# Kernel tuning notes

Hardware: AMD Instinct MI355X
Metric: run time of the kernel (lower is better)

Reference implementation:

```python
import jax, jax.numpy as jnp
import numpy as np

B, T, E, H = 4, 1024, 1024, 16
DH = E // H  # 64
LTM, CM0, CM1, MEM = 1, 512, 256, 1024
KV = LTM + CM0 + CM1 + MEM + T  # 2817


def _shift(x):
    # relative-position shift trick; x: [..., i, j] -> [..., i, j]
    *pre, i, j = x.shape
    x = jnp.concatenate([x, jnp.zeros((*pre, i, i), x.dtype)], axis=-1)
    l = i + j - 1
    x = x.reshape(*pre, -1)
    pad = (-x.shape[-1]) % l
    x = jnp.concatenate([x, jnp.zeros((*pre, pad), x.dtype)], axis=-1)
    x = x.reshape(*pre, -1, l)
    return x[..., :i, i - 1:]


def setup_inputs() -> dict:
    key = jax.random.key(0)
    ks = jax.random.split(key, 10)
    return {
        'x': jax.random.normal(ks[0], (B, T, E), jnp.float32),
        'mem': jax.random.normal(ks[1], (B, MEM, E), jnp.float32),
        'cmem0': jax.random.normal(ks[2], (B, CM0, E), jnp.float32),
        'cmem1': jax.random.normal(ks[3], (B, CM1, E), jnp.float32),
        'ltmem': jax.random.normal(ks[4], (B, LTM, E), jnp.float32),
        'pos_emb': jax.random.normal(ks[5], (H, KV, DH), jnp.float32) * 0.02,
        'Wq': jax.random.normal(ks[6], (E, E), jnp.float32) * 0.02,
        'Wkv': jax.random.normal(ks[7], (2 * E, E), jnp.float32) * 0.02,
        'Wout': jax.random.normal(ks[8], (E, E), jnp.float32) * 0.02,
        'bout': jnp.zeros((E,), jnp.float32),
    }


def reference(x, mem, cmem0, cmem1, ltmem, pos_emb, Wq, Wkv, Wout, bout):
    b, t, e = x.shape
    scale = DH ** -0.5
    # kv input: (ltmem, *cmems, mem, x) along sequence dim
    kv_input = jnp.concatenate([ltmem, cmem0, cmem1, mem, x], axis=1)
    kv_len = kv_input.shape[1]
    total_mem_len = kv_len - t

    q = x @ Wq.T                       # [b, t, e]
    kv = kv_input @ Wkv.T              # [b, kv, 2e]
    k, v = jnp.split(kv, 2, axis=-1)

    mh = lambda z: z.reshape(b, -1, H, DH).transpose(0, 2, 1, 3)  # [b,h,n,dh]
    q, k, v = mh(q), mh(k), mh(v)

    dots = jnp.einsum('bhid,bhjd->bhij', q, k) * scale

    # relative positional contribution with shift trick
    pos = pos_emb[:, -kv_len:].astype(q.dtype)           # [h, kv, dh]
    pos_dots = jnp.einsum('bhid,hjd->bhij', q, pos) * scale
    pos_dots = _shift(pos_dots)                          # [b,h,t,kv]
    dots = dots + pos_dots

    # causal mask over current-segment queries; memories fully visible
    mask_value = -jnp.finfo(dots.dtype).max
    causal = jnp.triu(jnp.ones((t, kv_len), bool), k=1 + total_mem_len)
    dots = jnp.where(causal[None, None], mask_value, dots)

    attn = jax.nn.softmax(dots, axis=-1)
    out = jnp.einsum('bhij,bhjd->bhid', attn, v)
    out = out.transpose(0, 2, 1, 3).reshape(b, t, e)
    logits = out @ Wout.T + bout
    return logits
```

## Files before the change

kernel.cpp:

```cpp
#include <hip/hip_runtime.h>
#include <hip/hip_bf16.h>

#define B_    4
#define T_    1024
#define E_    1024
#define H_    16
#define DH_   64
#define KV_   2817
#define KVP_  2880
#define MEML_ 1793
#define POSP_ 3200
#define SC2_  0.18033688011112042f

typedef __attribute__((ext_vector_type(4))) float f32x4;
typedef __attribute__((ext_vector_type(8))) short bf8;
typedef __attribute__((ext_vector_type(4))) unsigned short u16x4;
typedef __attribute__((ext_vector_type(8))) unsigned short u16x8;
typedef unsigned short u16;

static __device__ __forceinline__ u16 f2b(float f) {
  union { __hip_bfloat16 b; u16 s; } u;
  u.b = __float2bfloat16(f);
  return u.s;
}

static __device__ __forceinline__ void gl_lds16(const void* g, void* l) {
  __builtin_amdgcn_global_load_lds(
      (const __attribute__((address_space(1))) unsigned int*)g,
      (__attribute__((address_space(3))) unsigned int*)l, 16, 0, 0);
}

static __device__ __forceinline__ f32x4 mfma16(bf8 a, bf8 b, f32x4 c) {
  return __builtin_amdgcn_mfma_f32_16x16x32_bf16(a, b, c, 0, 0, 0);
}


__global__ void k_build_kvin(const float* __restrict__ x, const float* __restrict__ mem,
                             const float* __restrict__ cm0, const float* __restrict__ cm1,
                             const float* __restrict__ ltm, u16* __restrict__ kvin)
{
  int idx = blockIdx.x * 256 + threadIdx.x;
  if (idx >= B_ * KV_ * 256) return;
  int e4 = idx & 255;
  int jt = idx >> 8;
  int b = jt / KV_;
  int j = jt - b * KV_;
  const float* src;
  if (j < 1)          src = ltm + (long)b * E_;
  else if (j < 513)   src = cm0 + ((long)b * 512 + (j - 1)) * E_;
  else if (j < 769)   src = cm1 + ((long)b * 256 + (j - 513)) * E_;
  else if (j < 1793)  src = mem + ((long)b * 1024 + (j - 769)) * E_;
  else                src = x   + ((long)b * 1024 + (j - 1793)) * E_;
  float4 v = ((const float4*)src)[e4];
  u16x4 o; o[0] = f2b(v.x); o[1] = f2b(v.y); o[2] = f2b(v.z); o[3] = f2b(v.w);
  *(u16x4*)(kvin + (long)jt * E_ + e4 * 4) = o;
}

__global__ void k_f2b4(const float* __restrict__ s, u16* __restrict__ d, int n4)
{
  int i = blockIdx.x * 256 + threadIdx.x;
  if (i >= n4) return;
  float4 v = ((const float4*)s)[i];
  u16x4 o; o[0] = f2b(v.x); o[1] = f2b(v.y); o[2] = f2b(v.z); o[3] = f2b(v.w);
  *(u16x4*)(d + (long)i * 4) = o;
}

__global__ void k_posb(const float* __restrict__ pos, u16* __restrict__ pb)
{
  int idx = blockIdx.x * 256 + threadIdx.x;
  if (idx >= H_ * POSP_ * 16) return;
  int e4 = idx & 15;
  int rest = idx >> 4;
  int m = rest % POSP_;
  int h = rest / POSP_;
  u16x4 o;
  if (m < KV_) {
    float4 v = ((const float4*)(pos + ((long)h * KV_ + m) * DH_))[e4];
    o[0] = f2b(v.x); o[1] = f2b(v.y); o[2] = f2b(v.z); o[3] = f2b(v.w);
  } else {
    o[0] = 0; o[1] = 0; o[2] = 0; o[3] = 0;
  }
  *(u16x4*)(pb + ((long)h * POSP_ + m) * DH_ + e4 * 4) = o;
}

__global__ void k_zeropad(u16* __restrict__ kb, u16* __restrict__ vb)
{
  int idx = blockIdx.x * 256 + threadIdx.x;
  const int NK = 64 * 63 * 64;
  if (idx < NK) {
    int bh = idx / (63 * 64);
    int r  = idx - bh * (63 * 64);
    int j  = 2817 + (r >> 6);
    int d  = r & 63;
    kb[((long)bh * KVP_ + j) * DH_ + d] = 0;
  } else if (idx < 2 * NK) {
    int i2 = idx - NK;
    int bh = i2 / (63 * 64);
    int r  = i2 - bh * (63 * 64);
    int j  = 2817 + (r >> 6);
    int d  = r & 63;
    vb[((long)bh * KVP_ + j) * DH_ + d] = 0;
  }
}

__global__ __launch_bounds__(256)
void k_vtrans(const u16* __restrict__ vb, u16* __restrict__ vtb)
{
  __shared__ u16 tile[64][66];
  const int bh = blockIdx.y;
  const int j0 = blockIdx.x * 64;
  const u16* src = vb + ((long)bh * KVP_ + j0) * DH_;
  u16* dst = vtb + (long)bh * DH_ * KVP_ + j0;
  const int t = threadIdx.x;
#pragma unroll
  for (int c = 0; c < 2; ++c) {
    int lin = c * 256 + t;
    int r = lin >> 3, ch = (lin & 7) * 8;
    u16x8 v = *(const u16x8*)(src + (long)r * DH_ + ch);
    *(u16x4*)&tile[r][ch]     = *(const u16x4*)&v;
    *(u16x4*)&tile[r][ch + 4] = *(((const u16x4*)&v) + 1);
  }
  __syncthreads();
#pragma unroll
  for (int c = 0; c < 2; ++c) {
    int lin = c * 256 + t;
    int d = lin >> 3, jc = (lin & 7) * 8;
    u16x8 o;
#pragma unroll
    for (int e = 0; e < 8; ++e) o[e] = tile[jc + e][d];
    *(u16x8*)(dst + (long)d * KVP_ + jc) = o;
  }
}


template<int MODE>
__global__ __launch_bounds__(256)
void gemm_bt(const u16* __restrict__ A, const u16* __restrict__ Bw,
             u16* __restrict__ Out16, u16* __restrict__ Out16b,
             float* __restrict__ Outf, const float* __restrict__ bias)
{
  constexpr int Kd = 1024;
  constexpr int NT = (MODE == 1) ? 16 : 8;
  __shared__ u16 As[128 * 32];
  __shared__ u16 Bs[128 * 32];
  const int bid = blockIdx.x;
  const int mt = bid / NT, ntl = bid - mt * NT;
  const int m0 = mt * 128, n0 = ntl * 128;
  const int t = threadIdx.x;
  const int w = t >> 6, lane = t & 63;
  const int wr = w >> 1, wc = w & 1;
  const int l15 = lane & 15, lg = lane >> 4;
  const int xr = l15 & 3;
  const int xo = (lg ^ xr) << 4;

  f32x4 c00{}, c01{}, c02{}, c03{}, c10{}, c11{}, c12{}, c13{},
        c20{}, c21{}, c22{}, c23{}, c30{}, c31{}, c32{}, c33{};

  long growA[2]; int nrowB[2], xcA[2];
#pragma unroll
  for (int c = 0; c < 2; ++c) {
    int lin = c * 256 + t;
    int row = lin >> 2;
    xcA[c] = ((lin & 3) ^ (row & 3)) * 8;
    int m = m0 + row;
    long grow;
    if (MODE == 0)      { int b = m >> 10; grow = (long)b * KV_ + MEML_ + (m & 1023); }
    else if (MODE == 1) { grow = (m > 11267) ? 11267 : m; }
    else                { grow = m; }
    growA[c] = grow;
    nrowB[c] = n0 + row;
  }

  const char* pa = (const char*)As + (wr * 64 + l15) * 64 + xo;
  const char* pb = (const char*)Bs + (wc * 64 + l15) * 64 + xo;

  for (int kt = 0; kt < Kd; kt += 32) {
#pragma unroll
    for (int c = 0; c < 2; ++c) {
      int lin = c * 256 + t;
      gl_lds16(A + growA[c] * Kd + kt + xcA[c], (char*)As + lin * 16);
      gl_lds16(Bw + (long)nrowB[c] * Kd + kt + xcA[c], (char*)Bs + lin * 16);
    }
    __syncthreads();
    bf8 a0 = *(const bf8*)(pa);
    bf8 a1 = *(const bf8*)(pa + 16 * 64);
    bf8 a2 = *(const bf8*)(pa + 32 * 64);
    bf8 a3 = *(const bf8*)(pa + 48 * 64);
    bf8 b0 = *(const bf8*)(pb);
    bf8 b1 = *(const bf8*)(pb + 16 * 64);
    bf8 b2 = *(const bf8*)(pb + 32 * 64);
    bf8 b3 = *(const bf8*)(pb + 48 * 64);
    c00 = mfma16(a0, b0, c00); c01 = mfma16(a0, b1, c01);
    c02 = mfma16(a0, b2, c02); c03 = mfma16(a0, b3, c03);
    c10 = mfma16(a1, b0, c10); c11 = mfma16(a1, b1, c11);
    c12 = mfma16(a1, b2, c12); c13 = mfma16(a1, b3, c13);
    c20 = mfma16(a2, b0, c20); c21 = mfma16(a2, b1, c21);
    c22 = mfma16(a2, b2, c22); c23 = mfma16(a2, b3, c23);
    c30 = mfma16(a3, b0, c30); c31 = mfma16(a3, b1, c31);
    c32 = mfma16(a3, b2, c32); c33 = mfma16(a3, b3, c33);
    __syncthreads();
  }

  auto epi = [&](int mi, int ni, f32x4 ac) {
    int mb = m0 + wr * 64 + mi * 16 + lg * 4;
    int n  = n0 + wc * 64 + ni * 16 + l15;
    if (MODE == 0) {
      int hh = n >> 6, d = n & 63;
#pragma unroll
      for (int g = 0; g < 4; ++g) {
        int m = mb + g; int b = m >> 10, tq = m & 1023;
        Out16[((long)(b * 16 + hh) * T_ + tq) * DH_ + d] = f2b(ac[g]);
      }
    } else if (MODE == 1) {
      if (n < 1024) {
        int hh = n >> 6, d = n & 63;
#pragma unroll
        for (int g = 0; g < 4; ++g) {
          int m = mb + g; if (m >= 11268) continue;
          int b = m / KV_, j = m - b * KV_;
          Out16[((long)(b * 16 + hh) * KVP_ + j) * DH_ + d] = f2b(ac[g]);
        }
      } else {
        int n2 = n - 1024, hh = n2 >> 6, d = n2 & 63;
#pragma unroll
        for (int g = 0; g < 4; ++g) {
          int m = mb + g; if (m >= 11268) continue;
          int b = m / KV_, j = m - b * KV_;
          Out16b[((long)(b * 16 + hh) * KVP_ + j) * DH_ + d] = f2b(ac[g]);
        }
      }
    } else {
      float bv = bias[n];
#pragma unroll
      for (int g = 0; g < 4; ++g) {
        int m = mb + g;
        Outf[(long)m * E_ + n] = ac[g] + bv;
      }
    }
  };

  epi(0, 0, c00); epi(0, 1, c01); epi(0, 2, c02); epi(0, 3, c03);
  epi(1, 0, c10); epi(1, 1, c11); epi(1, 2, c12); epi(1, 3, c13);
  epi(2, 0, c20); epi(2, 1, c21); epi(2, 2, c22); epi(2, 3, c23);
  epi(3, 0, c30); epi(3, 1, c31); epi(3, 2, c32); epi(3, 3, c33);
}


__global__ __launch_bounds__(256)
void attn_kernel(const u16* __restrict__ Qb, const u16* __restrict__ Kb,
                 const u16* __restrict__ Vtb, const u16* __restrict__ Pb,
                 u16* __restrict__ Ob)
{
  __shared__ u16 Ks[64 * 64];
  __shared__ u16 Vs[64 * 64];
  __shared__ u16 Ps[128 * 64];
  __shared__ float Pg[4][16 * 84];

  const int i0 = blockIdx.x * 64;
  const int bh = blockIdx.y;
  const int h  = bh & 15;
  const int t  = threadIdx.x;
  const int w  = t >> 6, lane = t & 63;
  const int l15 = lane & 15, lg = lane >> 4, lk8 = lg * 8;
  const int iwb = i0 + w * 16;

  const u16* Qp = Qb + ((long)bh * T_ + i0) * DH_;
  const u16* Kp = Kb + (long)bh * KVP_ * DH_;
  const u16* Vp = Vtb + (long)bh * DH_ * KVP_;
  const u16* Pp = Pb + (long)h * POSP_ * DH_;
  float* Pgw = &Pg[w][0];

  bf8 qf0 = *(const bf8*)(Qp + (w * 16 + l15) * DH_ + lk8);
  bf8 qf1 = *(const bf8*)(Qp + (w * 16 + l15) * DH_ + 32 + lk8);

  f32x4 Oa[4] = {};
  float Mr[4] = {-1e30f, -1e30f, -1e30f, -1e30f};
  float Lr[4] = {0.f, 0.f, 0.f, 0.f};

  const int ntiles = (MEML_ + i0 + 63) / 64 + 1;

  for (int tl = 0; tl < ntiles; ++tl) {
    const int n0 = tl * 64;
    const int m0wg = n0 - i0 + 960;
#pragma unroll
    for (int c = 0; c < 2; ++c) {
      int lin = c * 256 + t; int row = lin >> 3; int sc = ((lin & 7) ^ (row & 7)) * 8;
      gl_lds16(Kp + (long)(n0 + row) * DH_ + sc, (char*)Ks + lin * 16);
    }
#pragma unroll
    for (int c = 0; c < 2; ++c) {
      int lin = c * 256 + t; int row = lin >> 3; int sc = ((lin & 7) ^ (row & 7)) * 8;
      gl_lds16(Vp + (long)row * KVP_ + n0 + sc, (char*)Vs + lin * 16);
    }
#pragma unroll
    for (int c = 0; c < 4; ++c) {
      int lin = c * 256 + t; int row = lin >> 3; int sc = ((lin & 7) ^ (row & 7)) * 8;
      gl_lds16(Pp + (long)(m0wg + row) * DH_ + sc, (char*)Ps + lin * 16);
    }
    __syncthreads();

    f32x4 sf[4];
#pragma unroll
    for (int cf = 0; cf < 4; ++cf) {
      int row = cf * 16 + l15;
      int x0 = (lk8 * 2) ^ ((row & 7) << 4);
      int x1 = (64 + lk8 * 2) ^ ((row & 7) << 4);
      f32x4 z = {0.f, 0.f, 0.f, 0.f};
      z = mfma16(qf0, *(const bf8*)((const char*)Ks + (row << 7) + x0), z);
      z = mfma16(qf1, *(const bf8*)((const char*)Ks + (row << 7) + x1), z);
      sf[cf] = z;
    }
#pragma unroll
    for (int pf = 0; pf < 5; ++pf) {
      int prow = pf * 16 + l15 + 48 - 16 * w;
      int x0 = (lk8 * 2) ^ ((prow & 7) << 4);
      int x1 = (64 + lk8 * 2) ^ ((prow & 7) << 4);
      f32x4 z = {0.f, 0.f, 0.f, 0.f};
      z = mfma16(qf0, *(const bf8*)((const char*)Ps + (prow << 7) + x0), z);
      z = mfma16(qf1, *(const bf8*)((const char*)Ps + (prow << 7) + x1), z);
#pragma unroll
      for (int g = 0; g < 4; ++g)
        Pgw[(lg * 4 + g) * 84 + pf * 16 + l15] = z[g];
    }
    float sv[4][4];
    const bool mm = (n0 + 63) > (MEML_ + iwb);
#pragma unroll
    for (int cf = 0; cf < 4; ++cf) {
      int c = cf * 16 + l15;
#pragma unroll
      for (int g = 0; g < 4; ++g) {
        int r = lg * 4 + g;
        float pv = Pgw[r * 84 + (c + 15 - r)];
        float s2 = (sf[cf][g] + pv) * SC2_;
        if (mm && (n0 + c) > (MEML_ + iwb + r)) s2 = -1e30f;
        sv[cf][g] = s2;
      }
    }
#pragma unroll
    for (int g = 0; g < 4; ++g) {
      float v = fmaxf(fmaxf(sv[0][g], sv[1][g]), fmaxf(sv[2][g], sv[3][g]));
      v = fmaxf(v, __shfl_xor(v, 1)); v = fmaxf(v, __shfl_xor(v, 2));
      v = fmaxf(v, __shfl_xor(v, 4)); v = fmaxf(v, __shfl_xor(v, 8));
      float Mn = fmaxf(Mr[g], v);
      float corr = exp2f(Mr[g] - Mn);
      Mr[g] = Mn;
      float p0 = exp2f(sv[0][g] - Mn), p1 = exp2f(sv[1][g] - Mn);
      float p2 = exp2f(sv[2][g] - Mn), p3 = exp2f(sv[3][g] - Mn);
      float ls = p0 + p1 + p2 + p3;
      ls += __shfl_xor(ls, 1); ls += __shfl_xor(ls, 2);
      ls += __shfl_xor(ls, 4); ls += __shfl_xor(ls, 8);
      Lr[g] = Lr[g] * corr + ls;
#pragma unroll
      for (int of = 0; of < 4; ++of) Oa[of][g] *= corr;
      int r = lg * 4 + g;
      Pgw[r * 84 + l15]      = p0;
      Pgw[r * 84 + 16 + l15] = p1;
      Pgw[r * 84 + 32 + l15] = p2;
      Pgw[r * 84 + 48 + l15] = p3;
    }
#pragma unroll
    for (int ks = 0; ks < 2; ++ks) {
      f32x4 a0 = *(const f32x4*)&Pgw[l15 * 84 + ks * 32 + lk8];
      f32x4 a1 = *(const f32x4*)&Pgw[l15 * 84 + ks * 32 + lk8 + 4];
      bf8 pa;
      pa[0] = (short)f2b(a0[0]); pa[1] = (short)f2b(a0[1]);
      pa[2] = (short)f2b(a0[2]); pa[3] = (short)f2b(a0[3]);
      pa[4] = (short)f2b(a1[0]); pa[5] = (short)f2b(a1[1]);
      pa[6] = (short)f2b(a1[2]); pa[7] = (short)f2b(a1[3]);
#pragma unroll
      for (int vf = 0; vf < 4; ++vf) {
        int vrow = vf * 16 + l15;
        int xo = (ks * 64 + lk8 * 2) ^ ((vrow & 7) << 4);
        bf8 vb_ = *(const bf8*)((const char*)Vs + (vrow << 7) + xo);
        Oa[vf] = mfma16(pa, vb_, Oa[vf]);
      }
    }
    __syncthreads();
  }

#pragma unroll
  for (int vf = 0; vf < 4; ++vf)
#pragma unroll
    for (int g = 0; g < 4; ++g) {
      int r = lg * 4 + g;
      int ig = i0 + w * 16 + r;
      float v = Oa[vf][g] / Lr[g];
      Ob[((long)(bh >> 4) * T_ + ig) * E_ + h * DH_ + vf * 16 + l15] = f2b(v);
    }
}


extern "C" void kernel_launch(void* const* d_in, const int* in_sizes, int n_in,
                              void* d_out, int out_size, void* d_ws, size_t ws_size,
                              hipStream_t stream)
{
  const float* x    = (const float*)d_in[0];
  const float* mem  = (const float*)d_in[1];
  const float* cm0  = (const float*)d_in[2];
  const float* cm1  = (const float*)d_in[3];
  const float* ltm  = (const float*)d_in[4];
  const float* pos  = (const float*)d_in[5];
  const float* Wq   = (const float*)d_in[6];
  const float* Wkv  = (const float*)d_in[7];
  const float* Wout = (const float*)d_in[8];
  const float* bout = (const float*)d_in[9];

  char* ws = (char*)d_ws;
  u16* kvin  = (u16*)(ws + 0);
  u16* vtb   = (u16*)(ws + 0);
  u16* wq_b  = (u16*)(ws + 23076864);
  u16* wkv_b = (u16*)(ws + 25174016);
  u16* wout_b= (u16*)(ws + 29368320);
  u16* posb  = (u16*)(ws + 31465472);
  u16* qb    = (u16*)(ws + 38019072);
  u16* kb    = (u16*)(ws + 46407680);
  u16* vb    = (u16*)(ws + 70000640);
  u16* ob    = (u16*)(ws + 93593600);

  k_build_kvin<<<11268, 256, 0, stream>>>(x, mem, cm0, cm1, ltm, kvin);
  k_f2b4<<<1024, 256, 0, stream>>>(Wq, wq_b, 262144);
  k_f2b4<<<2048, 256, 0, stream>>>(Wkv, wkv_b, 524288);
  k_f2b4<<<1024, 256, 0, stream>>>(Wout, wout_b, 262144);
  k_posb<<<3200, 256, 0, stream>>>(pos, posb);
  k_zeropad<<<2016, 256, 0, stream>>>(kb, vb);

  gemm_bt<0><<<256, 256, 0, stream>>>(kvin, wq_b, qb, nullptr, nullptr, nullptr);
  gemm_bt<1><<<1424, 256, 0, stream>>>(kvin, wkv_b, kb, vb, nullptr, nullptr);
  k_vtrans<<<dim3(45, 64), 256, 0, stream>>>(vb, vtb);
  attn_kernel<<<dim3(16, 64), 256, 0, stream>>>(qb, kb, vtb, posb, ob);
  gemm_bt<2><<<256, 256, 0, stream>>>(ob, wout_b, nullptr, nullptr, (float*)d_out, bout);
}
```

Baseline: 563.0 us.

## Double-buffer K/V tiles, load positional fragments into registers, reverse block order

After: 531.8 us. -5.5%, faster.

```diff
diff --git a/kernel.cpp b/kernel.cpp
--- a/kernel.cpp
+++ b/kernel.cpp
@@ -246,17 +246,16 @@
 }
 
 
-__global__ __launch_bounds__(256)
+__global__ __launch_bounds__(256, 3)
 void attn_kernel(const u16* __restrict__ Qb, const u16* __restrict__ Kb,
                  const u16* __restrict__ Vtb, const u16* __restrict__ Pb,
                  u16* __restrict__ Ob)
 {
-  __shared__ u16 Ks[64 * 64];
-  __shared__ u16 Vs[64 * 64];
-  __shared__ u16 Ps[128 * 64];
+  __shared__ u16 Ks[2][64 * 64];
+  __shared__ u16 Vs[2][64 * 64];
   __shared__ float Pg[4][16 * 84];
 
-  const int i0 = blockIdx.x * 64;
+  const int i0 = (15 - blockIdx.x) * 64;
   const int bh = blockIdx.y;
   const int h  = bh & 15;
   const int t  = threadIdx.x;
@@ -277,27 +276,47 @@
   float Mr[4] = {-1e30f, -1e30f, -1e30f, -1e30f};
   float Lr[4] = {0.f, 0.f, 0.f, 0.f};
 
-  const int ntiles = (MEML_ + i0 + 63) / 64 + 1;
-
-  for (int tl = 0; tl < ntiles; ++tl) {
-    const int n0 = tl * 64;
-    const int m0wg = n0 - i0 + 960;
+  const int ntiles = 30 + (i0 >> 6);
+
+  auto STAGE = [&](int tl, int bsel) {
+    const int n0s = tl * 64;
 #pragma unroll
     for (int c = 0; c < 2; ++c) {
       int lin = c * 256 + t; int row = lin >> 3; int sc = ((lin & 7) ^ (row & 7)) * 8;
-      gl_lds16(Kp + (long)(n0 + row) * DH_ + sc, (char*)Ks + lin * 16);
+      gl_lds16(Kp + (long)(n0s + row) * DH_ + sc, (char*)&Ks[bsel][0] + lin * 16);
     }
 #pragma unroll
     for (int c = 0; c < 2; ++c) {
       int lin = c * 256 + t; int row = lin >> 3; int sc = ((lin & 7) ^ (row & 7)) * 8;
-      gl_lds16(Vp + (long)row * KVP_ + n0 + sc, (char*)Vs + lin * 16);
-    }
-#pragma unroll
-    for (int c = 0; c < 4; ++c) {
-      int lin = c * 256 + t; int row = lin >> 3; int sc = ((lin & 7) ^ (row & 7)) * 8;
-      gl_lds16(Pp + (long)(m0wg + row) * DH_ + sc, (char*)Ps + lin * 16);
-    }
-    __syncthreads();
+      gl_lds16(Vp + (long)row * KVP_ + n0s + sc, (char*)&Vs[bsel][0] + lin * 16);
+    }
+  };
+
+  bf8 p00, p01, p10, p11, p20, p21, p30, p31, p40, p41;
+  auto POSLOAD = [&](int tl) {
+    const u16* pp = Pp + (long)(tl * 64 - i0 + 1008 - 16 * w + l15) * DH_ + lk8;
+    p00 = *(const bf8*)(pp);             p01 = *(const bf8*)(pp + 32);
+    p10 = *(const bf8*)(pp + 16 * DH_);  p11 = *(const bf8*)(pp + 16 * DH_ + 32);
+    p20 = *(const bf8*)(pp + 32 * DH_);  p21 = *(const bf8*)(pp + 32 * DH_ + 32);
+    p30 = *(const bf8*)(pp + 48 * DH_);  p31 = *(const bf8*)(pp + 48 * DH_ + 32);
+    p40 = *(const bf8*)(pp + 64 * DH_);  p41 = *(const bf8*)(pp + 64 * DH_ + 32);
+  };
+
+  STAGE(0, 0);
+  __builtin_amdgcn_sched_barrier(0);
+  POSLOAD(0);
+  asm volatile("s_waitcnt vmcnt(10)" ::: "memory");
+  __builtin_amdgcn_s_barrier();
+
+  for (int tl = 0; tl < ntiles; ++tl) {
+    const int bsel = tl & 1;
+    const int n0 = tl * 64;
+    const bool more = (tl + 1 < ntiles);
+    if (more) STAGE(tl + 1, bsel ^ 1);
+    __builtin_amdgcn_sched_barrier(0);
+
+    const char* Kbase = (const char*)&Ks[bsel][0];
+    const char* Vbase = (const char*)&Vs[bsel][0];
 
     f32x4 sf[4];
 #pragma unroll
@@ -306,22 +325,31 @@
       int x0 = (lk8 * 2) ^ ((row & 7) << 4);
       int x1 = (64 + lk8 * 2) ^ ((row & 7) << 4);
       f32x4 z = {0.f, 0.f, 0.f, 0.f};
-      z = mfma16(qf0, *(const bf8*)((const char*)Ks + (row << 7) + x0), z);
-      z = mfma16(qf1, *(const bf8*)((const char*)Ks + (row << 7) + x1), z);
+      z = mfma16(qf0, *(const bf8*)(Kbase + (row << 7) + x0), z);
+      z = mfma16(qf1, *(const bf8*)(Kbase + (row << 7) + x1), z);
       sf[cf] = z;
     }
-#pragma unroll
-    for (int pf = 0; pf < 5; ++pf) {
-      int prow = pf * 16 + l15 + 48 - 16 * w;
-      int x0 = (lk8 * 2) ^ ((prow & 7) << 4);
-      int x1 = (64 + lk8 * 2) ^ ((prow & 7) << 4);
-      f32x4 z = {0.f, 0.f, 0.f, 0.f};
-      z = mfma16(qf0, *(const bf8*)((const char*)Ps + (prow << 7) + x0), z);
-      z = mfma16(qf1, *(const bf8*)((const char*)Ps + (prow << 7) + x1), z);
-#pragma unroll
-      for (int g = 0; g < 4; ++g)
-        Pgw[(lg * 4 + g) * 84 + pf * 16 + l15] = z[g];
-    }
+
+    {
+      f32x4 z0 = {0.f,0.f,0.f,0.f}, z1 = {0.f,0.f,0.f,0.f}, z2 = {0.f,0.f,0.f,0.f},
+            z3 = {0.f,0.f,0.f,0.f}, z4 = {0.f,0.f,0.f,0.f};
+      z0 = mfma16(qf0, p00, z0); z0 = mfma16(qf1, p01, z0);
+      z1 = mfma16(qf0, p10, z1); z1 = mfma16(qf1, p11, z1);
+      z2 = mfma16(qf0, p20, z2); z2 = mfma16(qf1, p21, z2);
+      z3 = mfma16(qf0, p30, z3); z3 = mfma16(qf1, p31, z3);
+      z4 = mfma16(qf0, p40, z4); z4 = mfma16(qf1, p41, z4);
+#pragma unroll
+      for (int g = 0; g < 4; ++g) {
+        int rb = (lg * 4 + g) * 84 + l15;
+        Pgw[rb]      = z0[g];
+        Pgw[rb + 16] = z1[g];
+        Pgw[rb + 32] = z2[g];
+        Pgw[rb + 48] = z3[g];
+        Pgw[rb + 64] = z4[g];
+      }
+    }
+    if (more) POSLOAD(tl + 1);
+
     float sv[4][4];
     const bool mm = (n0 + 63) > (MEML_ + iwb);
 #pragma unroll
@@ -371,11 +399,15 @@
       for (int vf = 0; vf < 4; ++vf) {
         int vrow = vf * 16 + l15;
         int xo = (ks * 64 + lk8 * 2) ^ ((vrow & 7) << 4);
-        bf8 vb_ = *(const bf8*)((const char*)Vs + (vrow << 7) + xo);
+        bf8 vb_ = *(const bf8*)(Vbase + (vrow << 7) + xo);
         Oa[vf] = mfma16(pa, vb_, Oa[vf]);
       }
     }
-    __syncthreads();
+
+    if (more) {
+      asm volatile("s_waitcnt vmcnt(10)" ::: "memory");
+      __builtin_amdgcn_s_barrier();
+    }
   }
 
 #pragma unroll
```
